# Optimization experiments

Hardware: AMD Instinct MI355X
Metric: run time of the kernel (lower is better)

Reference implementation:

```python
import jax, jax.numpy as jnp
import numpy as np

B, T, V, E, H, O = 32, 512, 32000, 512, 1024, 128


def setup_inputs() -> dict:
    key = jax.random.key(0)
    ks = jax.random.split(key, 8)
    s = lambda k, shape: (jax.random.normal(k, shape) * 0.02).astype(jnp.float32)
    return {
        "tokens": jax.random.randint(ks[0], (B, T), 0, V),
        "verb_indices": jax.random.randint(ks[1], (B,), 0, T),
        "emb": s(ks[2], (V, E)),
        "W_ih": s(ks[3], (4 * H, E)),
        "W_hh": s(ks[4], (4 * H, H)),
        "b_ih": jnp.zeros((4 * H,), jnp.float32),
        "b_hh": jnp.zeros((4 * H,), jnp.float32),
        "W_lin": s(ks[5], (O, 2 * H)),
        "b_lin": jnp.zeros((O,), jnp.float32),
    }


def _lstm(e, W_ih, W_hh, b_ih, b_hh):
    # e: [B,T,E] -> hidden states [B,T,H]; PyTorch gate order i,f,g,o
    Hd = W_hh.shape[1]
    # precompute input projections for all timesteps (one big GEMM)
    x_proj = jnp.einsum("bte,ge->btg", e, W_ih) + b_ih + b_hh  # [B,T,4H]

    def step(carry, x_t):
        h, c = carry
        gates = x_t + h @ W_hh.T  # [B,4H]
        i, f, g, o = jnp.split(gates, 4, axis=-1)
        i = jax.nn.sigmoid(i)
        f = jax.nn.sigmoid(f)
        g = jnp.tanh(g)
        o = jax.nn.sigmoid(o)
        c = f * c + i * g
        h = o * jnp.tanh(c)
        return (h, c), h

    h0 = jnp.zeros((e.shape[0], Hd), e.dtype)
    (_, _), hs = jax.lax.scan(step, (h0, h0), jnp.swapaxes(x_proj, 0, 1))
    return jnp.swapaxes(hs, 0, 1)  # [B,T,H]


def reference(tokens, verb_indices, emb, W_ih, W_hh, b_ih, b_hh, W_lin, b_lin):
    e = emb[tokens]  # [B,T,E]
    out = _lstm(e, W_ih, W_hh, b_ih, b_hh)  # [B,T,H]
    verbs = out[jnp.arange(out.shape[0]), verb_indices]  # [B,H] verb hidden state
    # linear over concat([verb, out_t]) == split the weight and sum two GEMMs
    Wv, Wo = jnp.split(W_lin, 2, axis=1)  # [O,H] each
    logits = (
        jnp.einsum("bh,oh->bo", verbs, Wv)[:, None, :]
        + jnp.einsum("bth,oh->bto", out, Wo)
        + b_lin
    )  # [B,T,O]
    return jax.nn.log_softmax(logits, axis=-1)
```

## Files before the change

### kernel.cpp

```cpp
#include <hip/hip_runtime.h>


typedef short s8v __attribute__((ext_vector_type(8)));
typedef float f4v __attribute__((ext_vector_type(4)));

#define WS_CNT_OFF   131072
#define WS_VROWS_OFF 139264
#define WS_VLOG_OFF  204800

__device__ __forceinline__ float b2f(unsigned short u) {
    union { unsigned int i; float f; } x; x.i = ((unsigned int)u) << 16; return x.f;
}
__device__ __forceinline__ unsigned short f2b(float f) {
    union { float f; unsigned int i; } x; x.f = f;
    unsigned int r = (x.i + 0x7fffu + ((x.i >> 16) & 1u)) >> 16;
    return (unsigned short)r;
}
__device__ __forceinline__ float blo(unsigned int u) {
    union { unsigned int i; float f; } x; x.i = u << 16; return x.f;
}
__device__ __forceinline__ float bhi(unsigned int u) {
    union { unsigned int i; float f; } x; x.i = u & 0xffff0000u; return x.f;
}

__global__ void init_kernel(unsigned int* ws) {
    int i = blockIdx.x * 256 + threadIdx.x;
    if (i < 34816) ws[i] = 0u;
}

__device__ __forceinline__ void project_cols(
    const short* hA, const float* __restrict__ Wr0, const float* __restrict__ Wr1,
    float* __restrict__ dout, int b0, int tproj, int w, int tid)
{
    const int pair = tid >> 4, p = tid & 15;
    const int b = pair >> 1, oc = pair & 1;
    const float* wr = oc ? Wr1 : Wr0;
    float acc = 0.f;
#pragma unroll
    for (int j = 0; j < 8; ++j) {
        int ko = j * 16 + p;
        const unsigned int* d = (const unsigned int*)&hA[(ko * 17 + b) * 8];
        const float* wk = wr + ko * 8;
        f4v w0 = *(const f4v*)wk, w1 = *(const f4v*)(wk + 4);
        unsigned int d0 = d[0], d1 = d[1], d2 = d[2], d3 = d[3];
        acc += blo(d0) * w0[0] + bhi(d0) * w0[1] + blo(d1) * w0[2] + bhi(d1) * w0[3]
             + blo(d2) * w1[0] + bhi(d2) * w1[1] + blo(d3) * w1[2] + bhi(d3) * w1[3];
    }
#pragma unroll
    for (int off = 1; off < 16; off <<= 1) acc += __shfl_xor(acc, off);
    if (p == 0)
        dout[((size_t)(b0 + b) * 512 + tproj) * 128 + 2 * w + oc] = acc;
}

__global__ __launch_bounds__(256, 1) void scan_kernel(
    const int* __restrict__ tokens,
    const int* __restrict__ vidx,
    const float* __restrict__ emb,
    const float* __restrict__ W_ih,
    const float* __restrict__ W_hh,
    const float* __restrict__ b_ih,
    const float* __restrict__ b_hh,
    const float* __restrict__ W_lin,
    unsigned short* __restrict__ hbuf,
    unsigned int* __restrict__ cnt,
    unsigned short* __restrict__ vrows,
    float* __restrict__ dout)
{
    __shared__ short hA[128 * 17 * 8];
    __shared__ short eA[64 * 17 * 8];
    __shared__ float gbuf[16 * 65];

    const int tid  = threadIdx.x;
    const int g    = blockIdx.x >> 6;
    const int w    = blockIdx.x & 63;
    const int b0   = g * 8;
    const int lane = tid & 63;
    const int v    = tid >> 6;
    const int q    = lane >> 4;
    const int c    = lane & 15;

    const float* Wr0 = W_lin + (size_t)(2 * w) * 2048 + 1024;
    const float* Wr1 = W_lin + (size_t)(2 * w + 1) * 2048 + 1024;

    const int n = ((c >> 2) * 1024) + 16 * w + 4 * v + (c & 3);
    s8v Bh[32], Be[16];
    {
        const float* rh = W_hh + (size_t)n * 1024;
#pragma unroll
        for (int ks = 0; ks < 32; ++ks) {
            const float* s = rh + ks * 32 + q * 8;
            f4v lo = *(const f4v*)s, hi = *(const f4v*)(s + 4);
            s8v f;
#pragma unroll
            for (int j = 0; j < 4; ++j) { f[j] = (short)f2b(lo[j]); f[j + 4] = (short)f2b(hi[j]); }
            Bh[ks] = f;
        }
        const float* re = W_ih + (size_t)n * 512;
#pragma unroll
        for (int ks = 0; ks < 16; ++ks) {
            const float* s = re + ks * 32 + q * 8;
            f4v lo = *(const f4v*)s, hi = *(const f4v*)(s + 4);
            s8v f;
#pragma unroll
            for (int j = 0; j < 4; ++j) { f[j] = (short)f2b(lo[j]); f[j + 4] = (short)f2b(hi[j]); }
            Be[ks] = f;
        }
    }

    const s8v zv = {0,0,0,0,0,0,0,0};
    for (int i = tid; i < 1024; i += 256) { int ko = i >> 3, r = 8 + (i & 7);
        *(s8v*)&hA[(ko * 17 + r) * 8] = zv; }
    for (int i = tid; i < 512; i += 256) { int ko = i >> 3, r = 8 + (i & 7);
        *(s8v*)&eA[(ko * 17 + r) * 8] = zv; }

    float cst0 = 0.f, cst1 = 0.f;
    float bi0 = 0, bf0 = 0, bg0 = 0, bo0 = 0, bi1 = 0, bf1 = 0, bg1 = 0, bo1 = 0;
    int tvb = -1;
    const int pb = tid >> 3, pj2 = tid & 7;
    if (tid < 64) {
        int n0 = 16 * w + 2 * pj2, n1 = n0 + 1;
        bi0 = b_ih[n0]        + b_hh[n0];        bi1 = b_ih[n1]        + b_hh[n1];
        bf0 = b_ih[1024 + n0] + b_hh[1024 + n0]; bf1 = b_ih[1024 + n1] + b_hh[1024 + n1];
        bg0 = b_ih[2048 + n0] + b_hh[2048 + n0]; bg1 = b_ih[2048 + n1] + b_hh[2048 + n1];
        bo0 = b_ih[3072 + n0] + b_hh[3072 + n0]; bo1 = b_ih[3072 + n1] + b_hh[3072 + n1];
        tvb = vidx[b0 + pb];
    }

    unsigned short* hb   = hbuf + g * 2 * 8192;
    unsigned int*   hb32 = (unsigned int*)hb;
    unsigned int*   mycnt = cnt + g * 512;
    const int dwidx = ((2 * w + (pj2 >> 2)) * 8 + pb) * 4 + (pj2 & 3);
    int rp = 0;
    __syncthreads();

    for (int t = 0; t < 512; ++t) {
        for (int i = tid; i < 512; i += 256) {
            int ko = i >> 3, b = i & 7;
            int tok = tokens[(b0 + b) * 512 + t];
            const float* s = emb + (size_t)tok * 512 + ko * 8;
            f4v lo = *(const f4v*)s, hi = *(const f4v*)(s + 4);
            s8v f;
#pragma unroll
            for (int j = 0; j < 4; ++j) { f[j] = (short)f2b(lo[j]); f[j + 4] = (short)f2b(hi[j]); }
            *(s8v*)&eA[(ko * 17 + b) * 8] = f;
        }

        if (t >= 2)
            project_cols(hA, Wr0, Wr1, dout, b0, t - 2, w, tid);

        __syncthreads();

        f4v ae = {0.f, 0.f, 0.f, 0.f};
#pragma unroll
        for (int ks = 0; ks < 16; ++ks) {
            s8v a = *(const s8v*)&eA[((ks * 4 + q) * 17 + c) * 8];
            ae = __builtin_amdgcn_mfma_f32_16x16x32_bf16(a, Be[ks], ae, 0, 0, 0);
        }

        if (t > 0) {
            while (__hip_atomic_load(&mycnt[t - 1], __ATOMIC_RELAXED,
                                     __HIP_MEMORY_SCOPE_AGENT) < 64u) {}
        }

        {
            const unsigned long long* src =
                (const unsigned long long*)(hb + rp * 8192);
#pragma unroll
            for (int it = 0; it < 8; ++it) {
                int j = it * 256 + tid;
                unsigned long long d = __hip_atomic_load(src + j, __ATOMIC_RELAXED,
                                                         __HIP_MEMORY_SCOPE_AGENT);
                int ko = j >> 4, b = (j >> 1) & 7, posq = (j & 1) << 2;
                *(unsigned long long*)&hA[(ko * 17 + b) * 8 + posq] = d;
            }
        }
        __syncthreads();

        f4v ah0 = {0.f, 0.f, 0.f, 0.f}, ah1 = {0.f, 0.f, 0.f, 0.f};
#pragma unroll
        for (int ks = 0; ks < 16; ++ks) {
            s8v a0 = *(const s8v*)&hA[((2 * ks) * 4 + q) * 17 * 8 + c * 8];
            s8v a1 = *(const s8v*)&hA[((2 * ks + 1) * 4 + q) * 17 * 8 + c * 8];
            ah0 = __builtin_amdgcn_mfma_f32_16x16x32_bf16(a0, Bh[2 * ks], ah0, 0, 0, 0);
            ah1 = __builtin_amdgcn_mfma_f32_16x16x32_bf16(a1, Bh[2 * ks + 1], ah1, 0, 0, 0);
        }

#pragma unroll
        for (int r = 0; r < 4; ++r)
            gbuf[(q * 4 + r) * 65 + v * 16 + c] = ae[r] + ah0[r] + ah1[r];
        __syncthreads();

        if (tid < 64) {
            float h0, h1;
            {
                int pj = 2 * pj2, base = (pj >> 2) * 16, cb = pj & 3;
                float xi = gbuf[pb * 65 + base + cb]      + bi0;
                float xf = gbuf[pb * 65 + base + 4 + cb]  + bf0;
                float xg = gbuf[pb * 65 + base + 8 + cb]  + bg0;
                float xo = gbuf[pb * 65 + base + 12 + cb] + bo0;
                float ig = 1.f / (1.f + __expf(-xi));
                float fg = 1.f / (1.f + __expf(-xf));
                float gg = 1.f - 2.f / (1.f + __expf(2.f * xg));
                float og = 1.f / (1.f + __expf(-xo));
                cst0 = fg * cst0 + ig * gg;
                h0 = og * (1.f - 2.f / (1.f + __expf(2.f * cst0)));
            }
            {
                int pj = 2 * pj2 + 1, base = (pj >> 2) * 16, cb = pj & 3;
                float xi = gbuf[pb * 65 + base + cb]      + bi1;
                float xf = gbuf[pb * 65 + base + 4 + cb]  + bf1;
                float xg = gbuf[pb * 65 + base + 8 + cb]  + bg1;
                float xo = gbuf[pb * 65 + base + 12 + cb] + bo1;
                float ig = 1.f / (1.f + __expf(-xi));
                float fg = 1.f / (1.f + __expf(-xf));
                float gg = 1.f - 2.f / (1.f + __expf(2.f * xg));
                float og = 1.f / (1.f + __expf(-xo));
                cst1 = fg * cst1 + ig * gg;
                h1 = og * (1.f - 2.f / (1.f + __expf(2.f * cst1)));
            }
            unsigned int pack = (unsigned int)f2b(h0) | ((unsigned int)f2b(h1) << 16);
            __hip_atomic_store(&hb32[(rp ^ 1) * 4096 + dwidx], pack,
                               __ATOMIC_RELAXED, __HIP_MEMORY_SCOPE_AGENT);
            if (t == tvb)
                *(unsigned int*)&vrows[(b0 + pb) * 1024 + 16 * w + 2 * pj2] = pack;
        }
        __syncthreads();

        if (tid == 0)
            __hip_atomic_fetch_add(&mycnt[t], 1u, __ATOMIC_RELAXED,
                                   __HIP_MEMORY_SCOPE_AGENT);
        rp ^= 1;
    }

    project_cols(hA, Wr0, Wr1, dout, b0, 510, w, tid);
    __syncthreads();
    while (__hip_atomic_load(&mycnt[511], __ATOMIC_RELAXED,
                             __HIP_MEMORY_SCOPE_AGENT) < 64u) {}
    {
        const unsigned long long* src = (const unsigned long long*)(hb + rp * 8192);
#pragma unroll
        for (int it = 0; it < 8; ++it) {
            int j = it * 256 + tid;
            unsigned long long d = __hip_atomic_load(src + j, __ATOMIC_RELAXED,
                                                     __HIP_MEMORY_SCOPE_AGENT);
            int ko = j >> 4, b = (j >> 1) & 7, posq = (j & 1) << 2;
            *(unsigned long long*)&hA[(ko * 17 + b) * 8 + posq] = d;
        }
    }
    __syncthreads();
    project_cols(hA, Wr0, Wr1, dout, b0, 511, w, tid);
}

__global__ void verb_kernel(const unsigned short* __restrict__ vrows,
                            const float* __restrict__ W_lin,
                            const float* __restrict__ b_lin,
                            float* __restrict__ vlog)
{
    __shared__ float vrow[1024];
    int b = blockIdx.x, tid = threadIdx.x;
    for (int i = tid; i < 1024; i += 256) vrow[i] = b2f(vrows[b * 1024 + i]);
    __syncthreads();
    if (tid < 128) {
        float acc = 0.f;
        const float* wr = W_lin + (size_t)tid * 2048;
        for (int h = 0; h < 1024; ++h) acc += vrow[h] * wr[h];
        vlog[b * 128 + tid] = acc + b_lin[tid];
    }
}

__global__ void softmax_kernel(float* __restrict__ dout,
                               const float* __restrict__ vlog)
{
    int tid = threadIdx.x;
    int grow = blockIdx.x * 32 + (tid >> 3);
    int part = tid & 7;
    int b = grow >> 9;
    float* pp = dout + (size_t)grow * 128 + part * 16;
    const float* vb = vlog + b * 128 + part * 16;
    float L[16];
#pragma unroll
    for (int i = 0; i < 16; ++i) L[i] = pp[i] + vb[i];
    float m = L[0];
#pragma unroll
    for (int i = 1; i < 16; ++i) m = fmaxf(m, L[i]);
    for (int off = 1; off < 8; off <<= 1) m = fmaxf(m, __shfl_xor(m, off));
    float s = 0.f;
#pragma unroll
    for (int i = 0; i < 16; ++i) s += expf(L[i] - m);
    for (int off = 1; off < 8; off <<= 1) s += __shfl_xor(s, off);
    float lz = m + logf(s);
#pragma unroll
    for (int i = 0; i < 16; ++i) pp[i] = L[i] - lz;
}

extern "C" void kernel_launch(void* const* d_in, const int* in_sizes, int n_in,
                              void* d_out, int out_size, void* d_ws, size_t ws_size,
                              hipStream_t stream) {
    const int*   tokens = (const int*)d_in[0];
    const int*   vidx   = (const int*)d_in[1];
    const float* emb    = (const float*)d_in[2];
    const float* W_ih   = (const float*)d_in[3];
    const float* W_hh   = (const float*)d_in[4];
    const float* b_ih   = (const float*)d_in[5];
    const float* b_hh   = (const float*)d_in[6];
    const float* W_lin  = (const float*)d_in[7];
    const float* b_lin  = (const float*)d_in[8];
    float* dout = (float*)d_out;

    char* ws = (char*)d_ws;
    unsigned short* hbuf  = (unsigned short*)ws;
    unsigned int*   cnt   = (unsigned int*)(ws + WS_CNT_OFF);
    unsigned short* vrows = (unsigned short*)(ws + WS_VROWS_OFF);
    float*          vlog  = (float*)(ws + WS_VLOG_OFF);

    init_kernel<<<136, 256, 0, stream>>>((unsigned int*)ws);
    scan_kernel<<<256, 256, 0, stream>>>(tokens, vidx, emb, W_ih, W_hh, b_ih, b_hh,
                                         W_lin, hbuf, cnt, vrows, dout);
    verb_kernel<<<32, 256, 0, stream>>>(vrows, W_lin, b_lin, vlog);
    softmax_kernel<<<512, 256, 0, stream>>>(dout, vlog);
}
```

Baseline: 3.461 ms.

## Replace per-step atomic counter barrier with per-block step flags polled wave-wide

The cross-block step barrier changes from a single fetch_add counter per timestep to a per-block flag array. Each block stores its completed step number, and waiters poll all 64 flags in parallel with a wave-wide __all check. The trailing __syncthreads is dropped: the writer wave drains its stores with s_waitcnt vmcnt(0) and then sets the flag. The aim is to cut atomic contention and the barrier latency on the serial recurrence critical path. In exchange it depends on relaxed-ordering visibility without explicit fences, and on the removed block barrier not being needed for the shared-memory reuse. A vectorised LDS load in project_cols is also added.

```diff
diff --git a/kernel.cpp b/kernel.cpp
--- a/kernel.cpp
+++ b/kernel.cpp
@@ -3,6 +3,7 @@
 
 typedef short s8v __attribute__((ext_vector_type(8)));
 typedef float f4v __attribute__((ext_vector_type(4)));
+typedef unsigned int u4v __attribute__((ext_vector_type(4)));
 
 #define WS_CNT_OFF   131072
 #define WS_VROWS_OFF 139264
@@ -39,7 +40,7 @@
 #pragma unroll
     for (int j = 0; j < 8; ++j) {
         int ko = j * 16 + p;
-        const unsigned int* d = (const unsigned int*)&hA[(ko * 17 + b) * 8];
+        u4v d = *(const u4v*)&hA[(ko * 17 + b) * 8];
         const float* wk = wr + ko * 8;
         f4v w0 = *(const f4v*)wk, w1 = *(const f4v*)(wk + 4);
         unsigned int d0 = d[0], d1 = d[1], d2 = d[2], d3 = d[3];
@@ -62,7 +63,7 @@
     const float* __restrict__ b_hh,
     const float* __restrict__ W_lin,
     unsigned short* __restrict__ hbuf,
-    unsigned int* __restrict__ cnt,
+    unsigned int* __restrict__ flags_all,
     unsigned short* __restrict__ vrows,
     float* __restrict__ dout)
 {
@@ -128,7 +129,7 @@
 
     unsigned short* hb   = hbuf + g * 2 * 8192;
     unsigned int*   hb32 = (unsigned int*)hb;
-    unsigned int*   mycnt = cnt + g * 512;
+    unsigned int*   gflags = flags_all + g * 128;
     const int dwidx = ((2 * w + (pj2 >> 2)) * 8 + pb) * 4 + (pj2 & 3);
     int rp = 0;
     __syncthreads();
@@ -158,8 +159,13 @@
         }
 
         if (t > 0) {
-            while (__hip_atomic_load(&mycnt[t - 1], __ATOMIC_RELAXED,
-                                     __HIP_MEMORY_SCOPE_AGENT) < 64u) {}
+            const unsigned tt = (unsigned)t;
+            for (;;) {
+                unsigned f = __hip_atomic_load(&gflags[lane], __ATOMIC_RELAXED,
+                                               __HIP_MEMORY_SCOPE_AGENT);
+                if (__all(f >= tt)) break;
+            }
+            asm volatile("" ::: "memory");
         }
 
         {
@@ -223,19 +229,22 @@
                                __ATOMIC_RELAXED, __HIP_MEMORY_SCOPE_AGENT);
             if (t == tvb)
                 *(unsigned int*)&vrows[(b0 + pb) * 1024 + 16 * w + 2 * pj2] = pack;
-        }
-        __syncthreads();
-
-        if (tid == 0)
-            __hip_atomic_fetch_add(&mycnt[t], 1u, __ATOMIC_RELAXED,
-                                   __HIP_MEMORY_SCOPE_AGENT);
+            asm volatile("s_waitcnt vmcnt(0)" ::: "memory");
+            if (tid == 0)
+                __hip_atomic_store(&gflags[w], (unsigned)(t + 1),
+                                   __ATOMIC_RELAXED, __HIP_MEMORY_SCOPE_AGENT);
+        }
         rp ^= 1;
     }
 
     project_cols(hA, Wr0, Wr1, dout, b0, 510, w, tid);
     __syncthreads();
-    while (__hip_atomic_load(&mycnt[511], __ATOMIC_RELAXED,
-                             __HIP_MEMORY_SCOPE_AGENT) < 64u) {}
+    for (;;) {
+        unsigned f = __hip_atomic_load(&gflags[lane], __ATOMIC_RELAXED,
+                                       __HIP_MEMORY_SCOPE_AGENT);
+        if (__all(f >= 512u)) break;
+    }
+    asm volatile("" ::: "memory");
     {
         const unsigned long long* src = (const unsigned long long*)(hb + rp * 8192);
 #pragma unroll
@@ -309,13 +318,13 @@
 
     char* ws = (char*)d_ws;
     unsigned short* hbuf  = (unsigned short*)ws;
-    unsigned int*   cnt   = (unsigned int*)(ws + WS_CNT_OFF);
+    unsigned int*   flags = (unsigned int*)(ws + WS_CNT_OFF);
     unsigned short* vrows = (unsigned short*)(ws + WS_VROWS_OFF);
     float*          vlog  = (float*)(ws + WS_VLOG_OFF);
 
     init_kernel<<<136, 256, 0, stream>>>((unsigned int*)ws);
     scan_kernel<<<256, 256, 0, stream>>>(tokens, vidx, emb, W_ih, W_hh, b_ih, b_hh,
-                                         W_lin, hbuf, cnt, vrows, dout);
+                                         W_lin, hbuf, flags, vrows, dout);
     verb_kernel<<<32, 256, 0, stream>>>(vrows, W_lin, b_lin, vlog);
     softmax_kernel<<<512, 256, 0, stream>>>(dout, vlog);
 }
```

Measured after the change: 3.548 ms. 1.03x slower.
